# Kernel optimization log

Measured on AMD Instinct MI355X. Metric: run time of the kernel, lower is better.

The kernel has to match this reference:

```python
import jax, jax.numpy as jnp
import numpy as np

N = 50000      # nodes
E = 600000     # edges
C = 32         # in_features (channels)
COUT = 32      # out_features
NB = 8         # n_basis
NS = 10        # n_species
H = 64         # radial MLP hidden
NPATH = 5      # uvu paths for l_max=1: (0,0,0),(0,1,1),(1,0,1),(1,1,0),(1,1,1)
AVG = 12.0     # avg_n_neighbors
RS = 1.6765324703310907  # rescaled SiLU constant


def _rescaled_silu(x):
    return RS * jax.nn.silu(x)


def setup_inputs() -> dict:
    key = jax.random.key(0)
    ks = jax.random.split(key, 16)
    return {
        'node_attrs': jax.random.uniform(ks[0], (N, NS), dtype=jnp.float32),
        'node_feats': jax.random.normal(ks[1], (N, C, 4), dtype=jnp.float32),
        'edge_attrs': jax.random.normal(ks[2], (E, 1, 4), dtype=jnp.float32),
        'edge_feats': jax.random.normal(ks[3], (E, NB), dtype=jnp.float32),
        'W_first': jax.random.normal(ks[4], (2, C, C), dtype=jnp.float32),
        'Wr0': jax.random.normal(ks[5], (H, NB), dtype=jnp.float32),
        'Wr1': jax.random.normal(ks[6], (H, H), dtype=jnp.float32),
        'Wr2': jax.random.normal(ks[7], (H, H), dtype=jnp.float32),
        'Wr3': jax.random.normal(ks[8], (NPATH * C, H), dtype=jnp.float32),
        'W_second0': jax.random.normal(ks[9], (COUT, 2 * C), dtype=jnp.float32),
        'W_second1': jax.random.normal(ks[10], (COUT, 3 * C), dtype=jnp.float32),
        'W_skip': jax.random.normal(ks[11], (2, C, NS, C), dtype=jnp.float32),
        'idx_i': jnp.sort(jax.random.randint(ks[12], (E,), 0, N)),
        'idx_j': jax.random.randint(ks[13], (E,), 0, N),
    }


def reference(node_attrs, node_feats, edge_attrs, edge_feats, W_first, Wr0, Wr1,
              Wr2, Wr3, W_second0, W_second1, W_skip, idx_i, idx_j):
    # ---- skip_tp: uvw tensor product with l=0 node_attrs (species-dependent mixing per l)
    sc0 = jnp.einsum('ncm,nv,cvw->nwm', node_feats[:, :, :1], node_attrs, W_skip[0]) / np.sqrt(C * NS)
    sc1 = jnp.einsum('ncm,nv,cvw->nwm', node_feats[:, :, 1:4], node_attrs, W_skip[1]) / np.sqrt(C * NS)
    sc = jnp.concatenate([sc0, sc1], axis=-1)  # [N, C, 4]

    # ---- linear_first: per-l channel mixing
    x0 = jnp.einsum('ncm,dc->ndm', node_feats[:, :, :1], W_first[0]) / np.sqrt(C)   # [N,C,1]
    x1 = jnp.einsum('ncm,dc->ndm', node_feats[:, :, 1:4], W_first[1]) / np.sqrt(C)  # [N,C,3]

    # ---- radial MLP: Linear+RescaledSiLU chain, last SiLU dropped
    h = _rescaled_silu(edge_feats @ Wr0.T / np.sqrt(NB))
    h = _rescaled_silu(h @ Wr1.T / np.sqrt(H))
    h = _rescaled_silu(h @ Wr2.T / np.sqrt(H))
    w = (h @ Wr3.T / np.sqrt(H)).reshape(E, NPATH, C)  # per-edge, per-path, per-channel weights

    # ---- gather sender features
    xj0 = x0[idx_j][:, :, 0]   # [E, C]
    xj1 = x1[idx_j]            # [E, C, 3]
    y0 = edge_attrs[:, 0, 0]   # [E]      l=0 harmonic
    y1 = edge_attrs[:, 0, 1:4] # [E, 3]   l=1 harmonic

    # ---- uvu weighted tensor product (l_max=1 CG: scalar mult, dot, cross)
    p0 = w[:, 0] * xj0 * y0[:, None]                                   # (0,0,0) -> l=0
    p1 = w[:, 1, :, None] * xj0[:, :, None] * y1[:, None, :]          # (0,1,1) -> l=1
    p2 = w[:, 2, :, None] * xj1 * y0[:, None, None]                   # (1,0,1) -> l=1
    p3 = w[:, 3] * jnp.einsum('ecm,em->ec', xj1, y1)                  # (1,1,0) -> l=0
    p4 = w[:, 4, :, None] * jnp.cross(xj1, y1[:, None, :])            # (1,1,1) -> l=1

    # ---- scatter-add messages to receivers
    seg = lambda m: jax.ops.segment_sum(m, idx_i, num_segments=N)
    msg0 = seg(jnp.stack([p0, p3], axis=1))  # [N, 2, C]
    msg1 = seg(jnp.stack([p1, p2, p4], axis=1))  # [N, 3, C, 3]

    # ---- linear_second: mix (paths x channels) -> out_features per l
    out0 = jnp.einsum('npc,dpc->nd', msg0, W_second0.reshape(COUT, 2, C)) / np.sqrt(2 * C)
    out1 = jnp.einsum('npcm,dpc->ndm', msg1, W_second1.reshape(COUT, 3, C)) / np.sqrt(3 * C)
    message = jnp.concatenate([out0[:, :, None], out1], axis=-1) / AVG  # [N, COUT, 4]
    return message, sc
```

## Files before the change

kernel.cpp:

```cpp
#include <hip/hip_runtime.h>
#include <math.h>

#define N_NODES 50000
#define N_EDGES 600000

constexpr float RS          = 1.6765324703310907f;
constexpr float INV_SQRT8   = 0.35355339059327373f;
constexpr float INV8        = 0.125f;
constexpr float INV_SQRT320 = 0.05590169943749474f;
constexpr float INV_SQRT32  = 0.17677669529663687f;
constexpr float INV_SQRT96  = 0.10206207261596575f;
constexpr float INV_AVG     = 1.0f / 12.0f;

constexpr size_t OFF_X     = 0;
constexpr size_t OFF_ROW   = 25600000;
constexpr size_t OFF_FRAG  = 25800064;
constexpr size_t OFF_FRAG2 = 25841024;
constexpr size_t OFF_W     = 25931136;

typedef __attribute__((ext_vector_type(8))) short bfrag;
typedef __attribute__((ext_vector_type(4))) float ffrag;

__device__ __forceinline__ float rsilu(float z) {
  float t = __builtin_amdgcn_exp2f(z * -1.44269504088896341f);
  return (RS * z) * __builtin_amdgcn_rcpf(1.0f + t);
}
__device__ __forceinline__ unsigned short f2bf(float x) {
  unsigned u = __float_as_uint(x);
  u += 0x7FFFu + ((u >> 16) & 1u);
  return (unsigned short)(u >> 16);
}
__device__ __forceinline__ float bf2f(unsigned short u) {
  return __uint_as_float(((unsigned)u) << 16);
}

__global__ __launch_bounds__(256) void k_rowstart(const int* __restrict__ idx_i,
                                                  int* __restrict__ row,
                                                  int E, int N) {
  int e = blockIdx.x * 256 + threadIdx.x;
  if (e >= E) return;
  int cur  = idx_i[e];
  int prev = (e == 0) ? -1 : idx_i[e - 1];
  for (int n = prev + 1; n <= cur; ++n) row[n] = e;
  if (e == E - 1) {
    for (int n = cur + 1; n <= N; ++n) row[n] = E;
  }
}

__global__ __launch_bounds__(256) void k_prep(const float* __restrict__ Wr0,
                                              const float* __restrict__ Wr1,
                                              const float* __restrict__ Wr2,
                                              const float* __restrict__ Wr3,
                                              unsigned short* __restrict__ frag) {
  int t = blockIdx.x * 256 + threadIdx.x;
  int f    = t >> 9;
  int lane = (t >> 3) & 63;
  int j    = t & 7;
  int n16  = lane & 15, quad = lane >> 4;
  float v;
  if (f < 4) {
    int d = f * 16 + n16, k = quad * 8 + j;
    v = (k < 8) ? Wr0[d * 8 + k] * INV_SQRT8 : 0.f;
  } else if (f < 12) {
    int ff = f - 4, ntile = ff >> 1, ks = ff & 1;
    int d = ntile * 16 + n16, k = ks * 32 + quad * 8 + j;
    v = Wr1[d * 64 + k] * INV8;
  } else if (f < 20) {
    int ff = f - 12, ntile = ff >> 1, ks = ff & 1;
    int d = ntile * 16 + n16, k = ks * 32 + quad * 8 + j;
    v = Wr2[d * 64 + k] * INV8;
  } else {
    int ff = f - 20, ntile = ff >> 1, ks = ff & 1;
    int d = ntile * 16 + n16, k = ks * 32 + quad * 8 + j;
    v = Wr3[d * 64 + k] * INV8;
  }
  frag[t] = f2bf(v);
}

__global__ __launch_bounds__(256) void k_prep2(const float* __restrict__ Wsk,
                                               const float* __restrict__ Wf,
                                               unsigned short* __restrict__ frag2) {
  int t = blockIdx.x * 256 + threadIdx.x;
  int f    = t >> 9;
  int lane = (t >> 3) & 63;
  int j    = t & 7;
  int n16  = lane & 15, quad = lane >> 4;
  int ks = f >> 3, nt = f & 7;
  int k   = ks * 32 + quad * 8 + j;
  int col = nt * 16 + n16;
  float v = 0.f;
  if (k < 320) {
    int vv = k >> 5, c = k & 31;
    if (col < 32)       v = Wsk[(c * 10 + vv) * 32 + col] * INV_SQRT320;
    else if (col < 64)  v = Wsk[((32 + c) * 10 + vv) * 32 + (col - 32)] * INV_SQRT320;
  } else {
    int c = k - 320;
    if (col >= 96)      v = Wf[1024 + (col - 96) * 32 + c] * INV_SQRT32;
    else if (col >= 64) v = Wf[(col - 64) * 32 + c] * INV_SQRT32;
  }
  frag2[t] = f2bf(v);
}

__global__ __launch_bounds__(256) void k_node_mfma(const float* __restrict__ attrs,
                                                   const float* __restrict__ feats,
                                                   const unsigned short* __restrict__ frag2,
                                                   float* __restrict__ out_sc,
                                                   float* __restrict__ x_ws) {
  int tid = threadIdx.x;
  int wave = tid >> 6, lane = tid & 63;
  int quad = lane >> 4, l16 = lane & 15;
  int nb = blockIdx.x * 32 + wave * 8;

  float featsF[2][8];
  float a[2][10];
#pragma unroll
  for (int mt = 0; mt < 2; ++mt) {
    int nodeA = nb + mt * 4 + (l16 >> 2);
    if (nodeA > N_NODES - 1) nodeA = N_NODES - 1;
    int m = l16 & 3;
#pragma unroll
    for (int j = 0; j < 8; ++j)
      featsF[mt][j] = feats[(size_t)nodeA * 128 + (quad * 8 + j) * 4 + m];
#pragma unroll
    for (int v = 0; v < 10; ++v) a[mt][v] = attrs[nodeA * 10 + v];
  }

  ffrag acc[2][8];
#pragma unroll
  for (int mt = 0; mt < 2; ++mt)
#pragma unroll
    for (int nt = 0; nt < 8; ++nt) acc[mt][nt] = (ffrag){0.f, 0.f, 0.f, 0.f};

#pragma unroll
  for (int ks = 0; ks < 11; ++ks) {
    bfrag Ab[2];
#pragma unroll
    for (int mt = 0; mt < 2; ++mt) {
      union { unsigned short s8[8]; bfrag v; } pk;
#pragma unroll
      for (int j = 0; j < 8; ++j) {
        float val = (ks < 10) ? a[mt][ks] * featsF[mt][j] : featsF[mt][j];
        pk.s8[j] = f2bf(val);
      }
      Ab[mt] = pk.v;
    }
#pragma unroll
    for (int nt = 0; nt < 8; ++nt) {
      bfrag B = *(const bfrag*)(frag2 + ((size_t)(ks * 8 + nt) * 64 + lane) * 8);
      acc[0][nt] = __builtin_amdgcn_mfma_f32_16x16x32_bf16(Ab[0], B, acc[0][nt], 0, 0, 0);
      acc[1][nt] = __builtin_amdgcn_mfma_f32_16x16x32_bf16(Ab[1], B, acc[1][nt], 0, 0, 0);
    }
  }

#pragma unroll
  for (int mt = 0; mt < 2; ++mt) {
    int node = nb + mt * 4 + quad;
    if (node < N_NODES) {
      float4 sc0 = {acc[mt][0][0], acc[mt][2][1], acc[mt][2][2], acc[mt][2][3]};
      float4 sc1 = {acc[mt][1][0], acc[mt][3][1], acc[mt][3][2], acc[mt][3][3]};
      float4 x0  = {acc[mt][4][0], acc[mt][6][1], acc[mt][6][2], acc[mt][6][3]};
      float4 x1  = {acc[mt][5][0], acc[mt][7][1], acc[mt][7][2], acc[mt][7][3]};
      ((float4*)out_sc)[(size_t)node * 32 + l16]      = sc0;
      ((float4*)out_sc)[(size_t)node * 32 + 16 + l16] = sc1;
      ((float4*)x_ws)[(size_t)node * 32 + l16]        = x0;
      ((float4*)x_ws)[(size_t)node * 32 + 16 + l16]   = x1;
    }
  }
}

#define MLP_M 128
__global__ __launch_bounds__(256) void k_mlp(const float* __restrict__ ef,
                                             const unsigned short* __restrict__ frag,
                                             unsigned short* __restrict__ w_out,
                                             int E) {
  __shared__ __align__(16) unsigned short H[4][32][168];
  int tid = threadIdx.x;
  int wave = tid >> 6, lane = tid & 63;
  int quad = lane >> 4, l16 = lane & 15;
  int m0 = blockIdx.x * MLP_M + wave * 32;
  unsigned short (*Hw)[168] = H[wave];

  bfrag a1[2];
#pragma unroll
  for (int mt = 0; mt < 2; ++mt) {
    float vals[8] = {0.f, 0.f, 0.f, 0.f, 0.f, 0.f, 0.f, 0.f};
    if (quad == 0) {
      int r = m0 + mt * 16 + l16;
      if (r > E - 1) r = E - 1;
      const float4* p = (const float4*)(ef + (size_t)r * 8);
      float4 u0 = p[0], u1 = p[1];
      vals[0] = u0.x; vals[1] = u0.y; vals[2] = u0.z; vals[3] = u0.w;
      vals[4] = u1.x; vals[5] = u1.y; vals[6] = u1.z; vals[7] = u1.w;
    }
    union { unsigned short s[8]; bfrag v; } pk;
#pragma unroll
    for (int j = 0; j < 8; ++j) pk.s[j] = f2bf(vals[j]);
    a1[mt] = pk.v;
  }
#pragma unroll
  for (int nt = 0; nt < 4; ++nt) {
    const bfrag* bp = (const bfrag*)(frag + ((size_t)(nt) * 64 + lane) * 8);
    bfrag b = *bp;
    ffrag acc0 = {0.f, 0.f, 0.f, 0.f}, acc1 = acc0;
    acc0 = __builtin_amdgcn_mfma_f32_16x16x32_bf16(a1[0], b, acc0, 0, 0, 0);
    acc1 = __builtin_amdgcn_mfma_f32_16x16x32_bf16(a1[1], b, acc1, 0, 0, 0);
#pragma unroll
    for (int r = 0; r < 4; ++r) {
      Hw[0 * 16 + quad * 4 + r][nt * 16 + l16] = f2bf(rsilu(acc0[r]));
      Hw[1 * 16 + quad * 4 + r][nt * 16 + l16] = f2bf(rsilu(acc1[r]));
    }
  }

  bfrag A[2][2];
#pragma unroll 1
  for (int L = 0; L < 2; ++L) {
    int fbase = 4 + L * 8;
#pragma unroll
    for (int mt = 0; mt < 2; ++mt)
#pragma unroll
      for (int ks = 0; ks < 2; ++ks)
        A[mt][ks] = *(const bfrag*)&Hw[mt * 16 + l16][ks * 32 + quad * 8];
#pragma unroll
    for (int nt = 0; nt < 4; ++nt) {
      ffrag acc0 = {0.f, 0.f, 0.f, 0.f}, acc1 = acc0;
#pragma unroll
      for (int ks = 0; ks < 2; ++ks) {
        bfrag b = *(const bfrag*)(frag + ((size_t)(fbase + nt * 2 + ks) * 64 + lane) * 8);
        acc0 = __builtin_amdgcn_mfma_f32_16x16x32_bf16(A[0][ks], b, acc0, 0, 0, 0);
        acc1 = __builtin_amdgcn_mfma_f32_16x16x32_bf16(A[1][ks], b, acc1, 0, 0, 0);
      }
#pragma unroll
      for (int r = 0; r < 4; ++r) {
        Hw[0 * 16 + quad * 4 + r][nt * 16 + l16] = f2bf(rsilu(acc0[r]));
        Hw[1 * 16 + quad * 4 + r][nt * 16 + l16] = f2bf(rsilu(acc1[r]));
      }
    }
  }

#pragma unroll
  for (int mt = 0; mt < 2; ++mt)
#pragma unroll
    for (int ks = 0; ks < 2; ++ks)
      A[mt][ks] = *(const bfrag*)&Hw[mt * 16 + l16][ks * 32 + quad * 8];
#pragma unroll 2
  for (int nt = 0; nt < 10; ++nt) {
    ffrag acc0 = {0.f, 0.f, 0.f, 0.f}, acc1 = acc0;
#pragma unroll
    for (int ks = 0; ks < 2; ++ks) {
      bfrag b = *(const bfrag*)(frag + ((size_t)(20 + nt * 2 + ks) * 64 + lane) * 8);
      acc0 = __builtin_amdgcn_mfma_f32_16x16x32_bf16(A[0][ks], b, acc0, 0, 0, 0);
      acc1 = __builtin_amdgcn_mfma_f32_16x16x32_bf16(A[1][ks], b, acc1, 0, 0, 0);
    }
    int col = nt * 16 + l16;
    int p = col >> 5, cc = col & 31;
    int ncol = (p < 4) ? ((p >> 1) * 64 + 2 * cc + (p & 1)) : (128 + cc);
#pragma unroll
    for (int r = 0; r < 4; ++r) {
      Hw[0 * 16 + quad * 4 + r][ncol] = f2bf(acc0[r]);
      Hw[1 * 16 + quad * 4 + r][ncol] = f2bf(acc1[r]);
    }
  }

  {
    int row = lane / 20, off = lane - row * 20;
    int grow_base = m0;
#pragma unroll 2
    for (int it = 0; it < 10; ++it) {
      int grow = grow_base + row;
      uint4 v = *(const uint4*)&Hw[row][off * 8];
      if (grow < E)
        *(uint4*)(w_out + (size_t)grow * 160 + off * 8) = v;
      off += 4;
      row += 3;
      if (off >= 20) { off -= 20; row += 1; }
    }
  }
}

__global__ __launch_bounds__(256) void k_msg(const unsigned short* __restrict__ w_ws,
                                             const float* __restrict__ x_ws,
                                             const float* __restrict__ ea,
                                             const int* __restrict__ idx_j,
                                             const int* __restrict__ row,
                                             const float* __restrict__ Ws0,
                                             const float* __restrict__ Ws1,
                                             float* __restrict__ out_msg) {
  __shared__ __align__(16) float msg[8][356];
  __shared__ float W0T[64 * 33];
  __shared__ float W1T[96 * 33];

  int tid = threadIdx.x;
  for (int t = tid; t < 2048; t += 256) {
    int d = t >> 6, k = t & 63;
    W0T[k * 33 + d] = Ws0[t];
  }
  for (int t = tid; t < 3072; t += 256) {
    int d = t / 96, k = t % 96;
    W1T[k * 33 + d] = Ws1[t];
  }

  int ln = tid >> 5, c = tid & 31;
  int n = blockIdx.x * 8 + ln;
  int e0 = row[n], e1 = row[n + 1];

  float m00 = 0.f, m01 = 0.f;
  float m10x = 0.f, m10y = 0.f, m10z = 0.f;
  float m11x = 0.f, m11y = 0.f, m11z = 0.f;
  float m12x = 0.f, m12y = 0.f, m12z = 0.f;

  for (int base = e0; base < e1; base += 32) {
    int rem = e1 - base;
    int cnt = rem < 32 ? rem : 32;
    int jidx = base + (c < cnt ? c : cnt - 1);
    int j_c = __builtin_nontemporal_load(idx_j + jidx);

    for (int b = 0; b < cnt; b += 4) {
      int mvalid = cnt - b;
      float4 xj[4], y4[4];
      unsigned d01[4], d23[4];
      unsigned short w4v[4];
#pragma unroll
      for (int t = 0; t < 4; ++t) {
        int tt = (t < mvalid) ? t : 0;
        int e = base + b + tt;
        int j = __shfl(j_c, b + tt, 32);
        xj[t] = ((const float4*)x_ws)[(size_t)j * 32 + c];
        y4[t] = ((const float4*)ea)[e];
        const char* wb = (const char*)w_ws + (size_t)e * 320;
        d01[t] = *(const unsigned*)(wb + 4 * c);
        d23[t] = *(const unsigned*)(wb + 128 + 4 * c);
        w4v[t] = *(const unsigned short*)(wb + 256 + 2 * c);
      }
#pragma unroll
      for (int t = 0; t < 4; ++t) {
        if (t < mvalid) {
          float w0 = __uint_as_float(d01[t] << 16);
          float w1 = __uint_as_float(d01[t] & 0xffff0000u);
          float w2 = __uint_as_float(d23[t] << 16);
          float w3 = __uint_as_float(d23[t] & 0xffff0000u);
          float w4 = bf2f(w4v[t]);
          float4 x4 = xj[t], yy = y4[t];
          m00 += w0 * x4.x * yy.x;
          m01 += w3 * (x4.y * yy.y + x4.z * yy.z + x4.w * yy.w);
          m10x += w1 * x4.x * yy.y;
          m10y += w1 * x4.x * yy.z;
          m10z += w1 * x4.x * yy.w;
          m11x += w2 * x4.y * yy.x;
          m11y += w2 * x4.z * yy.x;
          m11z += w2 * x4.w * yy.x;
          float cx = x4.z * yy.w - x4.w * yy.z;
          float cy = x4.w * yy.y - x4.y * yy.w;
          float cz = x4.y * yy.z - x4.z * yy.y;
          m12x += w4 * cx;
          m12y += w4 * cy;
          m12z += w4 * cz;
        }
      }
    }
  }

  msg[ln][c]      = m00;
  msg[ln][32 + c] = m01;
  msg[ln][64 + 0 * 96 +  0 + c] = m10x;
  msg[ln][64 + 0 * 96 + 32 + c] = m11x;
  msg[ln][64 + 0 * 96 + 64 + c] = m12x;
  msg[ln][64 + 1 * 96 +  0 + c] = m10y;
  msg[ln][64 + 1 * 96 + 32 + c] = m11y;
  msg[ln][64 + 1 * 96 + 64 + c] = m12y;
  msg[ln][64 + 2 * 96 +  0 + c] = m10z;
  msg[ln][64 + 2 * 96 + 32 + c] = m11z;
  msg[ln][64 + 2 * 96 + 64 + c] = m12z;
  __syncthreads();

  float o0 = 0.f;
#pragma unroll 4
  for (int k4 = 0; k4 < 16; ++k4) {
    float4 mk = *(const float4*)&msg[ln][4 * k4];
    o0 += mk.x * W0T[(4 * k4 + 0) * 33 + c];
    o0 += mk.y * W0T[(4 * k4 + 1) * 33 + c];
    o0 += mk.z * W0T[(4 * k4 + 2) * 33 + c];
    o0 += mk.w * W0T[(4 * k4 + 3) * 33 + c];
  }
  float o1x = 0.f, o1y = 0.f, o1z = 0.f;
#pragma unroll 4
  for (int k4 = 0; k4 < 24; ++k4) {
    float4 ax = *(const float4*)&msg[ln][64 + 0 * 96 + 4 * k4];
    float4 ay = *(const float4*)&msg[ln][64 + 1 * 96 + 4 * k4];
    float4 az = *(const float4*)&msg[ln][64 + 2 * 96 + 4 * k4];
#pragma unroll
    for (int i = 0; i < 4; ++i) {
      float wv = W1T[(4 * k4 + i) * 33 + c];
      float mx = (i == 0) ? ax.x : (i == 1) ? ax.y : (i == 2) ? ax.z : ax.w;
      float my = (i == 0) ? ay.x : (i == 1) ? ay.y : (i == 2) ? ay.z : ay.w;
      float mz = (i == 0) ? az.x : (i == 1) ? az.y : (i == 2) ? az.z : az.w;
      o1x += mx * wv;
      o1y += my * wv;
      o1z += mz * wv;
    }
  }
  float4 res = {o0 * INV8 * INV_AVG, o1x * INV_SQRT96 * INV_AVG,
                o1y * INV_SQRT96 * INV_AVG, o1z * INV_SQRT96 * INV_AVG};
  ((float4*)out_msg)[(size_t)n * 32 + c] = res;
}

extern "C" void kernel_launch(void* const* d_in, const int* in_sizes, int n_in,
                              void* d_out, int out_size, void* d_ws, size_t ws_size,
                              hipStream_t stream) {
  const float* node_attrs = (const float*)d_in[0];
  const float* node_feats = (const float*)d_in[1];
  const float* edge_attrs = (const float*)d_in[2];
  const float* edge_feats = (const float*)d_in[3];
  const float* W_first    = (const float*)d_in[4];
  const float* Wr0        = (const float*)d_in[5];
  const float* Wr1        = (const float*)d_in[6];
  const float* Wr2        = (const float*)d_in[7];
  const float* Wr3        = (const float*)d_in[8];
  const float* Ws0        = (const float*)d_in[9];
  const float* Ws1        = (const float*)d_in[10];
  const float* Wsk        = (const float*)d_in[11];
  const int*   idx_i      = (const int*)d_in[12];
  const int*   idx_j      = (const int*)d_in[13];
  float* out = (float*)d_out;

  char* ws = (char*)d_ws;
  float*          x_ws   = (float*)(ws + OFF_X);
  int*            rowp   = (int*)(ws + OFF_ROW);
  unsigned short* fragp  = (unsigned short*)(ws + OFF_FRAG);
  unsigned short* frag2p = (unsigned short*)(ws + OFF_FRAG2);
  unsigned short* w_ws   = (unsigned short*)(ws + OFF_W);

  k_rowstart<<<(N_EDGES + 255) / 256, 256, 0, stream>>>(idx_i, rowp, N_EDGES, N_NODES);
  k_prep<<<80, 256, 0, stream>>>(Wr0, Wr1, Wr2, Wr3, fragp);
  k_prep2<<<176, 256, 0, stream>>>(Wsk, W_first, frag2p);
  k_node_mfma<<<(N_NODES + 31) / 32, 256, 0, stream>>>(node_attrs, node_feats,
                                                       frag2p, out + 6400000, x_ws);
  k_mlp<<<(N_EDGES + MLP_M - 1) / MLP_M, 256, 0, stream>>>(edge_feats, fragp,
                                                           w_ws, N_EDGES);
  k_msg<<<N_NODES / 8, 256, 0, stream>>>(w_ws, x_ws, edge_attrs, idx_j, rowp,
                                         Ws0, Ws1, out);
}
```

Before: 345.1 us.

## Use bf16 MFMA for linear_second epilogue and drop shared weight staging

```diff
diff --git a/kernel.cpp b/kernel.cpp
--- a/kernel.cpp
+++ b/kernel.cpp
@@ -286,19 +286,8 @@
                                              const float* __restrict__ Ws1,
                                              float* __restrict__ out_msg) {
   __shared__ __align__(16) float msg[8][356];
-  __shared__ float W0T[64 * 33];
-  __shared__ float W1T[96 * 33];
 
   int tid = threadIdx.x;
-  for (int t = tid; t < 2048; t += 256) {
-    int d = t >> 6, k = t & 63;
-    W0T[k * 33 + d] = Ws0[t];
-  }
-  for (int t = tid; t < 3072; t += 256) {
-    int d = t / 96, k = t % 96;
-    W1T[k * 33 + d] = Ws1[t];
-  }
-
   int ln = tid >> 5, c = tid & 31;
   int n = blockIdx.x * 8 + ln;
   int e0 = row[n], e1 = row[n + 1];
@@ -372,35 +361,59 @@
   msg[ln][64 + 2 * 96 + 64 + c] = m12z;
   __syncthreads();
 
-  float o0 = 0.f;
-#pragma unroll 4
-  for (int k4 = 0; k4 < 16; ++k4) {
-    float4 mk = *(const float4*)&msg[ln][4 * k4];
-    o0 += mk.x * W0T[(4 * k4 + 0) * 33 + c];
-    o0 += mk.y * W0T[(4 * k4 + 1) * 33 + c];
-    o0 += mk.z * W0T[(4 * k4 + 2) * 33 + c];
-    o0 += mk.w * W0T[(4 * k4 + 3) * 33 + c];
-  }
-  float o1x = 0.f, o1y = 0.f, o1z = 0.f;
-#pragma unroll 4
-  for (int k4 = 0; k4 < 24; ++k4) {
-    float4 ax = *(const float4*)&msg[ln][64 + 0 * 96 + 4 * k4];
-    float4 ay = *(const float4*)&msg[ln][64 + 1 * 96 + 4 * k4];
-    float4 az = *(const float4*)&msg[ln][64 + 2 * 96 + 4 * k4];
-#pragma unroll
-    for (int i = 0; i < 4; ++i) {
-      float wv = W1T[(4 * k4 + i) * 33 + c];
-      float mx = (i == 0) ? ax.x : (i == 1) ? ax.y : (i == 2) ? ax.z : ax.w;
-      float my = (i == 0) ? ay.x : (i == 1) ? ay.y : (i == 2) ? ay.z : ay.w;
-      float mz = (i == 0) ? az.x : (i == 1) ? az.y : (i == 2) ? az.z : az.w;
-      o1x += mx * wv;
-      o1y += my * wv;
-      o1z += mz * wv;
-    }
-  }
-  float4 res = {o0 * INV8 * INV_AVG, o1x * INV_SQRT96 * INV_AVG,
-                o1y * INV_SQRT96 * INV_AVG, o1z * INV_SQRT96 * INV_AVG};
-  ((float4*)out_msg)[(size_t)n * 32 + c] = res;
+  int wv = tid >> 6;
+  int lane = tid & 63;
+  int quad = lane >> 4, l16 = lane & 15;
+  int nb = blockIdx.x * 8;
+
+  const float* WS   = (wv == 0) ? Ws0 : Ws1;
+  int   K      = (wv == 0) ? 64 : 96;
+  int   mbase  = (wv == 0) ? 0 : 64 + (wv - 1) * 96;
+  float oscale = (wv == 0) ? (INV8 * INV_AVG) : (INV_SQRT96 * INV_AVG);
+
+  ffrag acc0 = {0.f, 0.f, 0.f, 0.f}, acc1 = acc0;
+  const float* arow = &msg[l16 & 7][mbase + quad * 8];
+#pragma unroll 1
+  for (int ks = 0; ks < K; ks += 32) {
+    float4 a0 = *(const float4*)(arow + ks);
+    float4 a1 = *(const float4*)(arow + ks + 4);
+    union { unsigned short s[8]; bfrag v; } pa;
+    pa.s[0] = f2bf(a0.x); pa.s[1] = f2bf(a0.y); pa.s[2] = f2bf(a0.z); pa.s[3] = f2bf(a0.w);
+    pa.s[4] = f2bf(a1.x); pa.s[5] = f2bf(a1.y); pa.s[6] = f2bf(a1.z); pa.s[7] = f2bf(a1.w);
+
+    const float* bp0 = WS + (size_t)l16 * K + ks + quad * 8;
+    const float* bp1 = bp0 + (size_t)16 * K;
+    {
+      float4 b0 = *(const float4*)(bp0);
+      float4 b1 = *(const float4*)(bp0 + 4);
+      union { unsigned short s[8]; bfrag v; } pb;
+      pb.s[0] = f2bf(b0.x * oscale); pb.s[1] = f2bf(b0.y * oscale);
+      pb.s[2] = f2bf(b0.z * oscale); pb.s[3] = f2bf(b0.w * oscale);
+      pb.s[4] = f2bf(b1.x * oscale); pb.s[5] = f2bf(b1.y * oscale);
+      pb.s[6] = f2bf(b1.z * oscale); pb.s[7] = f2bf(b1.w * oscale);
+      acc0 = __builtin_amdgcn_mfma_f32_16x16x32_bf16(pa.v, pb.v, acc0, 0, 0, 0);
+    }
+    {
+      float4 b0 = *(const float4*)(bp1);
+      float4 b1 = *(const float4*)(bp1 + 4);
+      union { unsigned short s[8]; bfrag v; } pb;
+      pb.s[0] = f2bf(b0.x * oscale); pb.s[1] = f2bf(b0.y * oscale);
+      pb.s[2] = f2bf(b0.z * oscale); pb.s[3] = f2bf(b0.w * oscale);
+      pb.s[4] = f2bf(b1.x * oscale); pb.s[5] = f2bf(b1.y * oscale);
+      pb.s[6] = f2bf(b1.z * oscale); pb.s[7] = f2bf(b1.w * oscale);
+      acc1 = __builtin_amdgcn_mfma_f32_16x16x32_bf16(pa.v, pb.v, acc1, 0, 0, 0);
+    }
+  }
+
+#pragma unroll
+  for (int r = 0; r < 4; ++r) {
+    int rowv = quad * 4 + r;
+    if (rowv < 8) {
+      size_t base = (size_t)(nb + rowv) * 128 + (size_t)l16 * 4 + wv;
+      out_msg[base]      = acc0[r];
+      out_msg[base + 64] = acc1[r];
+    }
+  }
 }
 
 extern "C" void kernel_launch(void* const* d_in, const int* in_sizes, int n_in,
```

Measured after the change: 333.7 us. 3.3% less time.
